# Optimization experiments

Measured on AMD Instinct MI355X. Metric: run time of the kernel, lower is better.

## Reference

```python
import jax, jax.numpy as jnp
import numpy as np

B, C, H, W = 2048, 32, 12, 12
N = H * W          # 144, fixed by pos_embed / relative_pos in GCNBlock
K = 9              # k-NN neighbors; dilation = 1


def _sincos_1d(d, pos):
    # standard 1D sin-cos embedding (ViG get_1d_sincos_pos_embed_from_grid)
    omega = np.arange(d // 2, dtype=np.float32) / (d / 2.0)
    omega = 1.0 / 10000 ** omega
    out = np.einsum('m,d->md', pos.astype(np.float32), omega)
    return np.concatenate([np.sin(out), np.cos(out)], axis=1)


def _relative_pos_table(dim, grid_size):
    # ViG get_2d_relative_pos_embed; Grapher stores the NEGATED table as a
    # frozen buffer that is ADDED to the pairwise distances before top-k.
    gw, gh = np.meshgrid(np.arange(grid_size, dtype=np.float32),
                         np.arange(grid_size, dtype=np.float32))
    pe = np.concatenate([_sincos_1d(dim // 2, gw.reshape(-1)),
                         _sincos_1d(dim // 2, gh.reshape(-1))], axis=1)  # (N, dim)
    rel = 2.0 * pe @ pe.T / pe.shape[1]
    return (-rel[None]).astype(np.float32)  # (1, N, N); n == HW so no interpolation


def setup_inputs() -> dict:
    key = jax.random.key(0)
    ks = jax.random.split(key, 8)
    def w(k, o, i):  # kaiming-normal per model_init
        return jax.random.normal(k, (o, i), jnp.float32) * (2.0 / i) ** 0.5
    z = lambda n: jnp.zeros((n,), jnp.float32)  # biases zeroed per model_init
    return {
        'inputs': jax.random.normal(ks[0], (B, C, H, W), jnp.float32),
        'pos_embed': jax.random.normal(ks[1], (1, C, H, W), jnp.float32) * 0.02,
        'relative_pos': jnp.asarray(_relative_pos_table(C, H)),
        'g_fc1_w': w(ks[2], C, C),       'g_fc1_b': z(C),
        'g_conv_w': w(ks[3], 2 * C, 2 * C), 'g_conv_b': z(2 * C),
        'g_fc2_w': w(ks[4], C, 2 * C),   'g_fc2_b': z(C),
        'f_fc1_w': w(ks[5], C, C),       'f_fc1_b': z(C),
        'f_fc2_w': w(ks[6], C, C),       'f_fc2_b': z(C),
    }


def _conv1x1(x, w, b):  # x: (B, Cin, H, W), w: (Cout, Cin)
    return jnp.einsum('bchw,oc->bohw', x, w) + b[None, :, None, None]


def _forward(inputs, pos_embed, relative_pos,
             g_fc1_w, g_fc1_b, g_conv_w, g_conv_b, g_fc2_w, g_fc2_b,
             f_fc1_w, f_fc1_b, f_fc2_w, f_fc2_b):
    x = inputs + pos_embed
    # ---- Grapher_noBN ----
    tmp = x
    x1 = _conv1x1(x, g_fc1_w, g_fc1_b)
    b, c, h, w = x1.shape
    n = h * w
    xf = x1.reshape(b, c, n)  # (B, C, N) node features
    # dynamic k-NN graph (torch does this under no_grad; indices kill grads anyway)
    xn = xf / jnp.clip(jnp.linalg.norm(xf, axis=1, keepdims=True), 1e-12)
    xt = jnp.swapaxes(xn, 1, 2)                      # (B, N, C)
    sq = jnp.sum(xt * xt, axis=-1)                   # (B, N)
    dist = sq[:, :, None] - 2.0 * jnp.einsum('bnc,bmc->bnm', xt, xt) + sq[:, None, :]
    dist = dist + relative_pos                       # (B, N, N)
    _, idx = jax.lax.top_k(-dist, K)                 # (B, N, K) nearest neighbors
    # MRConv2d: max-relative aggregation
    x_j = jax.vmap(lambda f, i: f[:, i])(xf, idx)    # (B, C, N, K) gather neighbors
    m = jnp.max(x_j - xf[:, :, :, None], axis=-1)    # (B, C, N)
    # interleave [x, max_rel] along channels: (B,C,2,N) -> (B,2C,N,1)
    stacked = jnp.stack([xf, m], axis=2).reshape(b, 2 * c, n, 1)
    hc = jnp.einsum('bcnk,oc->bonk', stacked, g_conv_w) + g_conv_b[None, :, None, None]
    hc = jax.nn.gelu(hc, approximate=False)          # BasicConv act (nn.GELU)
    hc = hc.reshape(b, 2 * c, h, w)
    x = _conv1x1(hc, g_fc2_w, g_fc2_b)
    x = x + tmp                                      # DropPath = identity (eval)
    # ---- FFN ----
    sc = x
    x = _conv1x1(x, f_fc1_w, f_fc1_b)
    x = jax.nn.gelu(x, approximate=False)
    x = _conv1x1(x, f_fc2_w, f_fc2_b)
    return x + sc


def reference(inputs, pos_embed, relative_pos,
              g_fc1_w, g_fc1_b, g_conv_w, g_conv_b, g_fc2_w, g_fc2_b,
              f_fc1_w, f_fc1_b, f_fc2_w, f_fc2_b):
    return _forward(inputs, pos_embed, relative_pos,
                    g_fc1_w, g_fc1_b, g_conv_w, g_conv_b, g_fc2_w, g_fc2_b,
                    f_fc1_w, f_fc1_b, f_fc2_w, f_fc2_b)
```

## Files before the change

kernel.cpp:

```cpp
#include <hip/hip_runtime.h>
#include <math.h>

#define BATCH 2048
#define CH    32
#define NN    144
#define KNN   9
#define PAD   36
#define TPB   192

__device__ __forceinline__ float gelu_exact(float x) {
    return 0.5f * x * (1.0f + erff(x * 0.70710678118654752440f));
}

__global__ __launch_bounds__(TPB) void gcn_main(
        const float* __restrict__ xin,
        const float* __restrict__ pos,
        const float* __restrict__ rel,
        const float* __restrict__ W1,  const float* __restrict__ B1,
        const float* __restrict__ WC,  const float* __restrict__ BC,
        const float* __restrict__ W2,  const float* __restrict__ B2,
        const float* __restrict__ F1,  const float* __restrict__ FB1,
        const float* __restrict__ F2,  const float* __restrict__ FB2,
        float* __restrict__ out) {
    const int t = threadIdx.x;
    const int n = t;
    const long bb = blockIdx.x;

    __shared__ __align__(16) float  s_xfT[NN * PAD];
    __shared__ float2 s_sr[NN];

    const float* xb = xin + bb * (CH * NN) + n;
    const float* pb = pos + n;

    float xfn[CH];

    if (t < NN) {
        float tc[CH];
        #pragma unroll
        for (int c = 0; c < CH; ++c) tc[c] = xb[c * NN] + pb[c * NN];
        float sum = 0.f;
        #pragma unroll
        for (int o = 0; o < CH; ++o) {
            float acc = B1[o];
            #pragma unroll
            for (int c = 0; c < CH; ++c) acc += W1[o * CH + c] * tc[c];
            xfn[o] = acc;
            sum += acc * acc;
        }
        float4* xr = (float4*)&s_xfT[n * PAD];
        #pragma unroll
        for (int q = 0; q < 8; ++q)
            xr[q] = make_float4(xfn[4*q], xfn[4*q+1], xfn[4*q+2], xfn[4*q+3]);
        float r = 1.0f / fmaxf(sqrtf(sum), 1e-12f);
        s_sr[n] = make_float2(sum * r * r, r);
    }
    __syncthreads();
    if (t >= NN) return;

    const float sqn = s_sr[n].x;
    const float rn2 = 2.0f * s_sr[n].y;
    float bestd[KNN];
    int   besti[KNN];
    #pragma unroll
    for (int k = 0; k < KNN; ++k) { bestd[k] = INFINITY; besti[k] = 0; }

    const float* reln = rel + n * NN;
    for (int mb = 0; mb < NN / 16; ++mb) {
        float rl[16];
        const float4* rp = (const float4*)(reln + mb * 16);
        #pragma unroll
        for (int q = 0; q < 4; ++q) {
            float4 v = rp[q];
            rl[4*q] = v.x; rl[4*q+1] = v.y; rl[4*q+2] = v.z; rl[4*q+3] = v.w;
        }
        #pragma unroll
        for (int mm = 0; mm < 16; ++mm) {
            const int m = mb * 16 + mm;
            const float4* row = (const float4*)&s_xfT[m * PAD];
            float dot = 0.f;
            #pragma unroll
            for (int q = 0; q < 8; ++q) {
                float4 v = row[q];
                dot += xfn[4*q] * v.x + xfn[4*q+1] * v.y
                     + xfn[4*q+2] * v.z + xfn[4*q+3] * v.w;
            }
            float2 sr = s_sr[m];
            float d = (sqn + sr.x + rl[mm]) - rn2 * sr.y * dot;
            if (d < bestd[KNN - 1]) {
                bestd[KNN - 1] = d; besti[KNN - 1] = m;
                #pragma unroll
                for (int k = KNN - 1; k > 0; --k) {
                    if (bestd[k] < bestd[k - 1]) {
                        float td = bestd[k]; bestd[k] = bestd[k - 1]; bestd[k - 1] = td;
                        int   ti = besti[k]; besti[k] = besti[k - 1]; besti[k - 1] = ti;
                    }
                }
            }
        }
    }

    float x2r[CH];
    #pragma unroll
    for (int o = 0; o < CH; ++o) x2r[o] = B2[o] + xb[o * NN] + pb[o * NN];

    float mrel[CH];
    #pragma unroll
    for (int c = 0; c < CH; ++c) mrel[c] = -INFINITY;
    #pragma unroll
    for (int k = 0; k < KNN; ++k) {
        const float4* nr = (const float4*)&s_xfT[besti[k] * PAD];
        #pragma unroll
        for (int q = 0; q < 8; ++q) {
            float4 v = nr[q];
            mrel[4*q]   = fmaxf(mrel[4*q],   v.x);
            mrel[4*q+1] = fmaxf(mrel[4*q+1], v.y);
            mrel[4*q+2] = fmaxf(mrel[4*q+2], v.z);
            mrel[4*q+3] = fmaxf(mrel[4*q+3], v.w);
        }
    }
    #pragma unroll
    for (int c = 0; c < CH; ++c) mrel[c] -= xfn[c];

    #pragma unroll 2
    for (int j = 0; j < 2 * CH; ++j) {
        float acc = BC[j];
        const float* wr = WC + j * 2 * CH;
        #pragma unroll
        for (int c = 0; c < CH; ++c)
            acc += wr[2*c] * xfn[c] + wr[2*c + 1] * mrel[c];
        float h = gelu_exact(acc);
        #pragma unroll
        for (int o = 0; o < CH; ++o) x2r[o] += W2[o * 2 * CH + j] * h;
    }

    float yv[CH];
    #pragma unroll
    for (int o = 0; o < CH; ++o) {
        float acc = FB1[o];
        #pragma unroll
        for (int c = 0; c < CH; ++c) acc += F1[o * CH + c] * x2r[c];
        yv[o] = gelu_exact(acc);
    }
    float* ob = out + bb * (CH * NN) + n;
    #pragma unroll
    for (int o = 0; o < CH; ++o) {
        float acc = FB2[o];
        #pragma unroll
        for (int c = 0; c < CH; ++c) acc += F2[o * CH + c] * yv[c];
        ob[o * NN] = acc + x2r[o];
    }
}

extern "C" void kernel_launch(void* const* d_in, const int* in_sizes, int n_in,
                              void* d_out, int out_size, void* d_ws, size_t ws_size,
                              hipStream_t stream) {
    const float* xin = (const float*)d_in[0];
    const float* pos = (const float*)d_in[1];
    const float* rel = (const float*)d_in[2];
    const float* w1  = (const float*)d_in[3];
    const float* b1  = (const float*)d_in[4];
    const float* wc  = (const float*)d_in[5];
    const float* bc  = (const float*)d_in[6];
    const float* w2  = (const float*)d_in[7];
    const float* b2  = (const float*)d_in[8];
    const float* f1  = (const float*)d_in[9];
    const float* fb1 = (const float*)d_in[10];
    const float* f2  = (const float*)d_in[11];
    const float* fb2 = (const float*)d_in[12];
    float* out = (float*)d_out;

    dim3 grid(BATCH), blk(TPB);
    gcn_main<<<grid, blk, 0, stream>>>(xin, pos, rel,
                                       w1, b1, wc, bc, w2, b2,
                                       f1, fb1, f2, fb2, out);
}
```

Before: 544.3 us.

## Split dense tail into separate kernel using split-bf16 MFMA matmuls

The main kernel now stops after the k-NN max-relative step and writes the features and max-relative values to a workspace. A second kernel runs the graph-conv, fc2 and FFN matmuls with bf16x3 split-precision MFMA over LDS-staged tiles. It also runs spot checks against a scalar recomputation and falls back to the scalar path if any check fails. The aim is to move the heavy per-thread FMA tail onto matrix cores, at the cost of an extra launch, workspace traffic and the check overhead.

```diff
diff --git a/kernel.cpp b/kernel.cpp
--- a/kernel.cpp
+++ b/kernel.cpp
@@ -7,6 +7,10 @@
 #define KNN   9
 #define PAD   36
 #define TPB   192
+#define HCP   68
+
+typedef short s16x8 __attribute__((ext_vector_type(8)));
+typedef float f32x4 __attribute__((ext_vector_type(4)));
 
 __device__ __forceinline__ float gelu_exact(float x) {
     return 0.5f * x * (1.0f + erff(x * 0.70710678118654752440f));
@@ -21,7 +25,8 @@
         const float* __restrict__ W2,  const float* __restrict__ B2,
         const float* __restrict__ F1,  const float* __restrict__ FB1,
         const float* __restrict__ F2,  const float* __restrict__ FB2,
-        float* __restrict__ out) {
+        float* __restrict__ out,
+        float* __restrict__ ws, const int run_tail) {
     const int t = threadIdx.x;
     const int n = t;
     const long bb = blockIdx.x;
@@ -121,34 +126,327 @@
     #pragma unroll
     for (int c = 0; c < CH; ++c) mrel[c] -= xfn[c];
 
-    #pragma unroll 2
-    for (int j = 0; j < 2 * CH; ++j) {
-        float acc = BC[j];
-        const float* wr = WC + j * 2 * CH;
-        #pragma unroll
-        for (int c = 0; c < CH; ++c)
-            acc += wr[2*c] * xfn[c] + wr[2*c + 1] * mrel[c];
-        float h = gelu_exact(acc);
-        #pragma unroll
-        for (int o = 0; o < CH; ++o) x2r[o] += W2[o * 2 * CH + j] * h;
-    }
-
-    float yv[CH];
-    #pragma unroll
-    for (int o = 0; o < CH; ++o) {
-        float acc = FB1[o];
-        #pragma unroll
-        for (int c = 0; c < CH; ++c) acc += F1[o * CH + c] * x2r[c];
-        yv[o] = gelu_exact(acc);
+    if (run_tail) {
+        #pragma unroll 2
+        for (int j = 0; j < 2 * CH; ++j) {
+            float acc = BC[j];
+            const float* wr = WC + j * 2 * CH;
+            #pragma unroll
+            for (int c = 0; c < CH; ++c)
+                acc += wr[2*c] * xfn[c] + wr[2*c + 1] * mrel[c];
+            float h = gelu_exact(acc);
+            #pragma unroll
+            for (int o = 0; o < CH; ++o) x2r[o] += W2[o * 2 * CH + j] * h;
+        }
+
+        float yv[CH];
+        #pragma unroll
+        for (int o = 0; o < CH; ++o) {
+            float acc = FB1[o];
+            #pragma unroll
+            for (int c = 0; c < CH; ++c) acc += F1[o * CH + c] * x2r[c];
+            yv[o] = gelu_exact(acc);
+        }
+        float* ob = out + bb * (CH * NN) + n;
+        #pragma unroll
+        for (int o = 0; o < CH; ++o) {
+            float acc = FB2[o];
+            #pragma unroll
+            for (int c = 0; c < CH; ++c) acc += F2[o * CH + c] * yv[c];
+            ob[o * NN] = acc + x2r[o];
+        }
+    } else {
+        float* wsb = ws + bb * (2 * CH * NN) + n;
+        #pragma unroll
+        for (int o = 0; o < CH; ++o) {
+            wsb[o * NN]        = xfn[o];
+            wsb[(CH + o) * NN] = mrel[o];
+        }
+    }
+}
+
+__device__ __forceinline__ unsigned bf_hi(float f) {
+    unsigned u = __float_as_uint(f);
+    return (u + 0x7fffu + ((u >> 16) & 1u)) >> 16;
+}
+__device__ __forceinline__ float bf_up(unsigned h) { return __uint_as_float(h << 16); }
+__device__ __forceinline__ unsigned pack2(float f) {
+    unsigned h = bf_hi(f);
+    unsigned l = bf_hi(f - bf_up(h));
+    return h | (l << 16);
+}
+__device__ __forceinline__ float unpk(unsigned u) {
+    return bf_up(u & 0xffffu) + bf_up(u >> 16);
+}
+__device__ __forceinline__ void unpack8(const unsigned* p, s16x8& hi, s16x8& lo) {
+    const uint4* q = (const uint4*)p;
+    uint4 u0 = q[0], u1 = q[1];
+    unsigned w[8] = {u0.x, u0.y, u0.z, u0.w, u1.x, u1.y, u1.z, u1.w};
+    short h[8], l[8];
+    #pragma unroll
+    for (int e = 0; e < 8; ++e) { h[e] = (short)(w[e] & 0xffffu); l[e] = (short)(w[e] >> 16); }
+    hi = (s16x8){h[0], h[1], h[2], h[3], h[4], h[5], h[6], h[7]};
+    lo = (s16x8){l[0], l[1], l[2], l[3], l[4], l[5], l[6], l[7]};
+}
+__device__ __forceinline__ void split8(const float* p, s16x8& hi, s16x8& lo) {
+    const float4* q = (const float4*)p;
+    float4 v0 = q[0], v1 = q[1];
+    float f[8] = {v0.x, v0.y, v0.z, v0.w, v1.x, v1.y, v1.z, v1.w};
+    short h[8], l[8];
+    #pragma unroll
+    for (int e = 0; e < 8; ++e) {
+        unsigned a = bf_hi(f[e]);
+        h[e] = (short)a;
+        l[e] = (short)bf_hi(f[e] - bf_up(a));
+    }
+    hi = (s16x8){h[0], h[1], h[2], h[3], h[4], h[5], h[6], h[7]};
+    lo = (s16x8){l[0], l[1], l[2], l[3], l[4], l[5], l[6], l[7]};
+}
+#define MFMA3(acc, ah, al, bh, bl)                                              \
+    acc = __builtin_amdgcn_mfma_f32_16x16x32_bf16(ah, bh, acc, 0, 0, 0);        \
+    acc = __builtin_amdgcn_mfma_f32_16x16x32_bf16(ah, bl, acc, 0, 0, 0);        \
+    acc = __builtin_amdgcn_mfma_f32_16x16x32_bf16(al, bh, acc, 0, 0, 0);
+
+__global__ __launch_bounds__(TPB) void gcn_tail(
+        const float* __restrict__ xin, const float* __restrict__ pos,
+        const float* __restrict__ WC,  const float* __restrict__ BC,
+        const float* __restrict__ W2,  const float* __restrict__ B2,
+        const float* __restrict__ F1,  const float* __restrict__ FB1,
+        const float* __restrict__ F2,  const float* __restrict__ FB2,
+        const float* __restrict__ ws,  float* __restrict__ out) {
+    const int t = threadIdx.x;
+    const int n = t;
+    const long bb = blockIdx.x;
+
+    __shared__ __align__(16) unsigned s_pool[NN * HCP];
+    __shared__ float s_x2[NN * 33];
+    __shared__ int s_flag;
+
+    float xfn[CH], mrel[CH], x2r[CH];
+    if (t == 0) s_flag = 0;
+
+    const float* wsb = ws + bb * (2 * CH * NN) + n;
+    const float* xb  = xin + bb * (CH * NN) + n;
+    const float* pb  = pos + n;
+
+    if (t < NN) {
+        #pragma unroll
+        for (int o = 0; o < CH; ++o) {
+            xfn[o]  = wsb[o * NN];
+            mrel[o] = wsb[(CH + o) * NN];
+            x2r[o]  = B2[o] + xb[o * NN] + pb[o * NN];
+        }
+        unsigned* sr = s_pool + n * HCP;
+        #pragma unroll
+        for (int e = 0; e < CH; ++e) {
+            sr[2*e]     = pack2(xfn[e]);
+            sr[2*e + 1] = pack2(mrel[e]);
+        }
+        #pragma unroll
+        for (int o = 0; o < CH; ++o) s_x2[n * 33 + o] = x2r[o];
+    }
+    __syncthreads();
+
+    const int wv   = t >> 6;
+    const int lane = t & 63;
+    const int lr   = lane & 15;
+    const int lq   = lane >> 4;
+    const int koff = lq * 8;
+
+    f32x4 acc1[3][4];
+    #pragma unroll
+    for (int mt = 0; mt < 3; ++mt)
+        #pragma unroll
+        for (int nt = 0; nt < 4; ++nt) acc1[mt][nt] = (f32x4){0.f, 0.f, 0.f, 0.f};
+    #pragma unroll
+    for (int ks = 0; ks < 2; ++ks) {
+        s16x8 bh[4], bl[4];
+        #pragma unroll
+        for (int nt = 0; nt < 4; ++nt)
+            split8(&WC[(nt*16 + lr) * 64 + ks*32 + koff], bh[nt], bl[nt]);
+        #pragma unroll
+        for (int mt = 0; mt < 3; ++mt) {
+            s16x8 ah, al;
+            unpack8(s_pool + ((wv*3 + mt)*16 + lr) * HCP + ks*32 + koff, ah, al);
+            #pragma unroll
+            for (int nt = 0; nt < 4; ++nt) { MFMA3(acc1[mt][nt], ah, al, bh[nt], bl[nt]); }
+        }
+    }
+    __syncthreads();
+    #pragma unroll
+    for (int mt = 0; mt < 3; ++mt)
+        #pragma unroll
+        for (int nt = 0; nt < 4; ++nt)
+            #pragma unroll
+            for (int r = 0; r < 4; ++r) {
+                const int row = (wv*3 + mt)*16 + 4*lq + r;
+                const int col = nt*16 + lr;
+                s_pool[row * HCP + col] = pack2(gelu_exact(acc1[mt][nt][r] + BC[col]));
+            }
+    __syncthreads();
+    if (t < NN) {
+        const int jp = n & 63;
+        float a = BC[jp];
+        const float* wr = WC + jp * 2 * CH;
+        #pragma unroll
+        for (int c = 0; c < CH; ++c) a += wr[2*c] * xfn[c] + wr[2*c + 1] * mrel[c];
+        if (fabsf(gelu_exact(a) - unpk(s_pool[n * HCP + jp])) > 0.05f) s_flag = 1;
+    }
+    __syncthreads();
+
+    f32x4 acc2[3][2];
+    #pragma unroll
+    for (int mt = 0; mt < 3; ++mt)
+        #pragma unroll
+        for (int nt = 0; nt < 2; ++nt) acc2[mt][nt] = (f32x4){0.f, 0.f, 0.f, 0.f};
+    #pragma unroll
+    for (int ks = 0; ks < 2; ++ks) {
+        s16x8 bh[2], bl[2];
+        #pragma unroll
+        for (int nt = 0; nt < 2; ++nt)
+            split8(&W2[(nt*16 + lr) * 64 + ks*32 + koff], bh[nt], bl[nt]);
+        #pragma unroll
+        for (int mt = 0; mt < 3; ++mt) {
+            s16x8 ah, al;
+            unpack8(s_pool + ((wv*3 + mt)*16 + lr) * HCP + ks*32 + koff, ah, al);
+            #pragma unroll
+            for (int nt = 0; nt < 2; ++nt) { MFMA3(acc2[mt][nt], ah, al, bh[nt], bl[nt]); }
+        }
+    }
+    float x2f[3][2][4];
+    #pragma unroll
+    for (int mt = 0; mt < 3; ++mt)
+        #pragma unroll
+        for (int nt = 0; nt < 2; ++nt)
+            #pragma unroll
+            for (int r = 0; r < 4; ++r) {
+                const int row = (wv*3 + mt)*16 + 4*lq + r;
+                const int col = nt*16 + lr;
+                const float v = acc2[mt][nt][r] + s_x2[row * 33 + col];
+                x2f[mt][nt][r] = v;
+                s_x2[row * 33 + col] = v;
+            }
+    __syncthreads();
+    if (t < NN) {
+        const int op = n & 31;
+        float e = x2r[op];
+        #pragma unroll
+        for (int j = 0; j < 2 * CH; ++j) e += W2[op * 2 * CH + j] * unpk(s_pool[n * HCP + j]);
+        if (fabsf(e - s_x2[n * 33 + op]) > 0.1f) s_flag = 1;
+    }
+    __syncthreads();
+    #pragma unroll
+    for (int mt = 0; mt < 3; ++mt)
+        #pragma unroll
+        for (int nt = 0; nt < 2; ++nt)
+            #pragma unroll
+            for (int r = 0; r < 4; ++r)
+                s_pool[((wv*3 + mt)*16 + 4*lq + r) * HCP + nt*16 + lr] = pack2(x2f[mt][nt][r]);
+    __syncthreads();
+
+    f32x4 acc3[3][2];
+    #pragma unroll
+    for (int mt = 0; mt < 3; ++mt)
+        #pragma unroll
+        for (int nt = 0; nt < 2; ++nt) acc3[mt][nt] = (f32x4){0.f, 0.f, 0.f, 0.f};
+    {
+        s16x8 bh[2], bl[2];
+        #pragma unroll
+        for (int nt = 0; nt < 2; ++nt)
+            split8(&F1[(nt*16 + lr) * 32 + koff], bh[nt], bl[nt]);
+        #pragma unroll
+        for (int mt = 0; mt < 3; ++mt) {
+            s16x8 ah, al;
+            unpack8(s_pool + ((wv*3 + mt)*16 + lr) * HCP + koff, ah, al);
+            #pragma unroll
+            for (int nt = 0; nt < 2; ++nt) { MFMA3(acc3[mt][nt], ah, al, bh[nt], bl[nt]); }
+        }
+    }
+    #pragma unroll
+    for (int mt = 0; mt < 3; ++mt)
+        #pragma unroll
+        for (int nt = 0; nt < 2; ++nt)
+            #pragma unroll
+            for (int r = 0; r < 4; ++r) {
+                const int row = (wv*3 + mt)*16 + 4*lq + r;
+                const int col = nt*16 + lr;
+                s_pool[row * HCP + 32 + col] = pack2(gelu_exact(acc3[mt][nt][r] + FB1[col]));
+            }
+    __syncthreads();
+    if (t < NN) {
+        const int op = n & 31;
+        float e = FB1[op];
+        #pragma unroll
+        for (int c = 0; c < CH; ++c) e += F1[op * CH + c] * unpk(s_pool[n * HCP + c]);
+        if (fabsf(gelu_exact(e) - unpk(s_pool[n * HCP + 32 + op])) > 0.1f) s_flag = 1;
+    }
+
+    f32x4 acc4[3][2];
+    #pragma unroll
+    for (int mt = 0; mt < 3; ++mt)
+        #pragma unroll
+        for (int nt = 0; nt < 2; ++nt) acc4[mt][nt] = (f32x4){0.f, 0.f, 0.f, 0.f};
+    {
+        s16x8 bh[2], bl[2];
+        #pragma unroll
+        for (int nt = 0; nt < 2; ++nt)
+            split8(&F2[(nt*16 + lr) * 32 + koff], bh[nt], bl[nt]);
+        #pragma unroll
+        for (int mt = 0; mt < 3; ++mt) {
+            s16x8 ah, al;
+            unpack8(s_pool + ((wv*3 + mt)*16 + lr) * HCP + 32 + koff, ah, al);
+            #pragma unroll
+            for (int nt = 0; nt < 2; ++nt) { MFMA3(acc4[mt][nt], ah, al, bh[nt], bl[nt]); }
+        }
+    }
+    __syncthreads();
+    float* poolf = (float*)s_pool;
+    #pragma unroll
+    for (int mt = 0; mt < 3; ++mt)
+        #pragma unroll
+        for (int nt = 0; nt < 2; ++nt)
+            #pragma unroll
+            for (int r = 0; r < 4; ++r) {
+                const int row = (wv*3 + mt)*16 + 4*lq + r;
+                const int col = nt*16 + lr;
+                poolf[row * HCP + col] = acc4[mt][nt][r] + FB2[col] + s_x2[row * 33 + col];
+            }
+    __syncthreads();
+
+    if (t >= NN) return;
+    if (s_flag != 0) {
+        #pragma unroll 2
+        for (int j = 0; j < 2 * CH; ++j) {
+            float acc = BC[j];
+            const float* wr = WC + j * 2 * CH;
+            #pragma unroll
+            for (int c = 0; c < CH; ++c)
+                acc += wr[2*c] * xfn[c] + wr[2*c + 1] * mrel[c];
+            float h = gelu_exact(acc);
+            #pragma unroll
+            for (int o = 0; o < CH; ++o) x2r[o] += W2[o * 2 * CH + j] * h;
+        }
+        float yv[CH];
+        #pragma unroll
+        for (int o = 0; o < CH; ++o) {
+            float acc = FB1[o];
+            #pragma unroll
+            for (int c = 0; c < CH; ++c) acc += F1[o * CH + c] * x2r[c];
+            yv[o] = gelu_exact(acc);
+        }
+        float* ob = out + bb * (CH * NN) + n;
+        #pragma unroll
+        for (int o = 0; o < CH; ++o) {
+            float acc = FB2[o];
+            #pragma unroll
+            for (int c = 0; c < CH; ++c) acc += F2[o * CH + c] * yv[c];
+            ob[o * NN] = acc + x2r[o];
+        }
+        return;
     }
     float* ob = out + bb * (CH * NN) + n;
     #pragma unroll
-    for (int o = 0; o < CH; ++o) {
-        float acc = FB2[o];
-        #pragma unroll
-        for (int c = 0; c < CH; ++c) acc += F2[o * CH + c] * yv[c];
-        ob[o * NN] = acc + x2r[o];
-    }
+    for (int o = 0; o < CH; ++o) ob[o * NN] = poolf[n * HCP + o];
 }
 
 extern "C" void kernel_launch(void* const* d_in, const int* in_sizes, int n_in,
@@ -169,8 +467,18 @@
     const float* fb2 = (const float*)d_in[12];
     float* out = (float*)d_out;
 
+    const size_t need = (size_t)BATCH * (2 * CH) * NN * sizeof(float);
+    const int run_tail = (d_ws == nullptr || ws_size < need) ? 1 : 0;
+
     dim3 grid(BATCH), blk(TPB);
     gcn_main<<<grid, blk, 0, stream>>>(xin, pos, rel,
                                        w1, b1, wc, bc, w2, b2,
-                                       f1, fb1, f2, fb2, out);
-}
+                                       f1, fb1, f2, fb2, out,
+                                       (float*)d_ws, run_tail);
+    if (!run_tail) {
+        gcn_tail<<<grid, blk, 0, stream>>>(xin, pos,
+                                           wc, bc, w2, b2,
+                                           f1, fb1, f2, fb2,
+                                           (const float*)d_ws, out);
+    }
+}
```

New measurement: 458.8 us. -15.7%, faster.
